# Kernel tuning notes

Hardware: AMD Instinct MI355X
Metric: run time of the kernel (lower is better)

The kernel has to match this reference:

```python
import itertools
import jax, jax.numpy as jnp
import numpy as np

ALPHA = 1e-4   # mse/conn mixing
BETA = 0.1
DMAX = 20.0
NCAP = 10.0    # costs_n_cap
PCAP = 3.0     # costs_p_cap
W3D = 64       # 3D cube window (window_3d)
W2D = 32       # 2D MALIS window (window_2d, default)


def _dilate5(mask):
    # scipy binary_dilation, default cross structuring element, 5 iterations
    m = mask.astype(bool)
    for _ in range(5):
        p = np.pad(m, 1)
        m = p[1:-1, 1:-1] | p[:-2, 1:-1] | p[2:, 1:-1] | p[1:-1, :-2] | p[1:-1, 2:]
    return m


def _label8(mask):
    # skimage.measure.label on boolean mask: 8-connectivity, background=0
    H, W = mask.shape
    lbl = np.zeros((H, W), np.int64)
    parent = {}

    def find(x):
        while parent[x] != x:
            parent[x] = parent[parent[x]]
            x = parent[x]
        return x

    nxt = 1
    for i in range(H):
        for j in range(W):
            if not mask[i, j]:
                continue
            neigh = []
            for di, dj in ((-1, -1), (-1, 0), (-1, 1), (0, -1)):
                ii, jj = i + di, j + dj
                if 0 <= ii < H and 0 <= jj < W and mask[ii, jj]:
                    neigh.append(int(lbl[ii, jj]))
            if not neigh:
                lbl[i, j] = nxt
                parent[nxt] = nxt
                nxt += 1
            else:
                m0 = min(neigh)
                lbl[i, j] = m0
                for nb in neigh:
                    ra, rb = find(m0), find(nb)
                    if ra != rb:
                        parent[max(ra, rb)] = min(ra, rb)
    out = np.zeros_like(lbl)
    remap = {}
    c = 0
    for i in range(H):
        for j in range(W):
            if lbl[i, j] > 0:
                r = find(int(lbl[i, j]))
                if r not in remap:
                    c += 1
                    remap[r] = c
                out[i, j] = remap[r]
    return out


def _malis_edge_weights(seg, n1, n2, costs, pos):
    # MALIS union-find / Kruskal maximal-spanning-tree pair counting.
    # Edges processed in descending cost order. Background (seg==0) nodes
    # are not counted. pos=1: #same-label pairs merged; pos=0: #diff-label pairs.
    n = seg.size
    parent = list(range(n))

    def find(x):
        r = x
        while parent[r] != r:
            r = parent[r]
        while parent[x] != r:
            parent[x], x = r, parent[x]
        return r

    cnt = [({int(s): 1} if s > 0 else {}) for s in seg]
    tot = [1 if s > 0 else 0 for s in seg]
    w = np.zeros(costs.shape[0], np.float32)
    for e in np.argsort(-costs, kind="stable"):
        ra, rb = find(int(n1[e])), find(int(n2[e]))
        if ra == rb:
            continue
        ca, cb = cnt[ra], cnt[rb]
        if len(ca) > len(cb):
            ra, rb, ca, cb = rb, ra, cb, ca
        same = 0
        for l, v in ca.items():
            same += v * cb.get(l, 0)
        w[e] = float(same if pos else tot[ra] * tot[rb] - same)
        for l, v in ca.items():
            cb[l] = cb.get(l, 0) + v
        tot[rb] += tot[ra]
        parent[ra] = rb
        cnt[ra] = None
    return w


def _window_weights(pred2d, tgt2d):
    # numpy MALIS node weights for a [B,1,H,W] 2D projection
    B, C, H, W = pred2d.shape
    w = W2D
    wn = np.zeros(pred2d.shape, np.float32)
    wp = np.zeros(pred2d.shape, np.float32)
    idx = np.arange(w * w).reshape(w, w)
    n1 = np.concatenate([idx[:, :-1].ravel(), idx[:-1, :].ravel()])
    n2 = np.concatenate([idx[:, 1:].ravel(), idx[1:, :].ravel()])
    nh = w * (w - 1)
    for k in range(H // w):
        for j in range(W // w):
            p = pred2d[:, :, k*w:(k+1)*w, j*w:(j+1)*w]
            t = tgt2d[:, :, k*w:(k+1)*w, j*w:(j+1)*w]
            ch = (p[:, :, :, :-1] + p[:, :, :, 1:]).reshape(B, -1)
            cv = (p[:, :, :-1, :] + p[:, :, 1:, :]).reshape(B, -1)
            costs = np.concatenate([ch, cv], 1).astype(np.float32)
            gh = (t[:, :, :, :-1] + t[:, :, :, 1:]).reshape(B, -1)
            gv = (t[:, :, :-1, :] + t[:, :, 1:, :]).reshape(B, -1)
            gt = np.concatenate([gh, gv], 1).astype(np.float32)
            costs_n = costs.copy()
            costs_p = costs.copy()
            costs_n[gt > NCAP] = NCAP
            costs_p[gt < PCAP] = 0.0
            gt = np.minimum(gt, NCAP)
            for b in range(B):
                sg = _label8(~_dilate5(t[b, 0] == 0)).ravel()
                en = _malis_edge_weights(sg, n1, n2, costs_n[b], 0)
                ep = _malis_edge_weights(sg, n1, n2, costs_p[b], 1)
                sn = en.sum()
                if sn > 0:
                    en = en / sn
                sp = ep.sum()
                if sp > 0:
                    ep = ep / sp
                en[gt[b] >= PCAP] = 0.0
                ep[gt[b] < NCAP] = 0.0
                for ew, out in ((en, wn), (ep, wp)):
                    eh = ew[:nh].reshape(w, w - 1)
                    ev = ew[nh:].reshape(w - 1, w)
                    nwt = np.zeros((w, w), np.float32)
                    nwt[:, :-1] += eh
                    nwt[:, 1:] += eh
                    nwt[:-1, :] += ev
                    nwt[1:, :] += ev
                    out[b, 0, k*w:(k+1)*w, j*w:(j+1)*w] = nwt
    return wn, wp


def _precompute(pred_np, tgt_np):
    # host-side (detached) MALIS weight maps, exactly as the torch module
    B, C, H, W, D = pred_np.shape
    items = []
    for k, j, i in itertools.product(range(H // W3D), range(W // W3D), range(D // W3D)):
        sl = (slice(None), slice(None), slice(k*W3D, (k+1)*W3D),
              slice(j*W3D, (j+1)*W3D), slice(i*W3D, (i+1)*W3D))
        pc, tc = pred_np[sl], tgt_np[sl]
        for axis in (2, 3, 4):
            wn, wp = _window_weights(pc.min(axis=axis), tc.min(axis=axis))
            items.append((k, j, i, axis, jnp.asarray(wn), jnp.asarray(wp)))
    return items


def _loss(pred, target, items):
    mse = jnp.mean((pred - target) ** 2)
    conn = jnp.float32(0.0)
    for (k, j, i, axis, wn, wp) in items:
        pc = pred[:, :, k*W3D:(k+1)*W3D, j*W3D:(j+1)*W3D, i*W3D:(i+1)*W3D]
        proj = jnp.min(pc, axis=axis)  # [B,1,64,64]
        conn = conn + jnp.sum(proj**2 * wn + BETA * (DMAX - proj)**2 * wp)
    return (mse, jnp.float32(ALPHA) * conn)


def setup_inputs() -> dict:
    # synthetic distance-transform-like volumes (zeros on 'vessel' seeds)
    rng = np.random.default_rng(0)
    B, H = 4, 128
    g = np.arange(H, dtype=np.float32)
    zz, yy, xx = np.meshgrid(g, g, g, indexing="ij")
    tgt = np.empty((B, 1, H, H, H), np.float32)
    for b in range(B):
        pts = rng.uniform(0, H, size=(24, 3)).astype(np.float32)
        d = np.full((H, H, H), np.inf, np.float32)
        for p in pts:
            d = np.minimum(d, np.sqrt((zz - p[0])**2 + (yy - p[1])**2 + (xx - p[2])**2))
        tgt[b, 0] = np.floor(np.minimum(d, DMAX))
    pred = np.clip(tgt + 0.5 * rng.standard_normal(tgt.shape).astype(np.float32), 0.0, DMAX).astype(np.float32)
    return {"pred": jnp.asarray(pred), "target": jnp.asarray(tgt)}


def reference(pred, target):
    items = _precompute(np.asarray(pred), np.asarray(target))
    return _loss(pred, target, items)
```

## Files before the change

kernel.cpp:

```cpp
#include <hip/hip_runtime.h>

#define BLOCK 256
#define NNODE 1024
#define NH    992
#define NE    1984
#define NSORT 2048
#define LMAX  12
#define CHUNK 64
#define NPASS (NE / CHUNK)

typedef unsigned long long ull;

__device__ __forceinline__ void edge_nodes(int e, int& a, int& b) {
    if (e < NH) {
        int r = e / 31;
        int c = e - r * 31;
        a = (r << 5) + c;
        b = a + 1;
    } else {
        a = e - NH;
        b = a + 32;
    }
}

__device__ __forceinline__ int find_par(unsigned short* par, int x) {
    volatile unsigned short* vp = par;
    int r = x;
    int p = vp[r];
    while (p != r) { r = p; p = vp[r]; }
    int c = x;
    while (c != r) { const int nxt = vp[c]; vp[c] = (unsigned short)r; c = nxt; }
    return r;
}

__device__ __forceinline__ int dot16x4(ull a, ull b) {
    int s  = (int)(a & 0xFFFFu)         * (int)(b & 0xFFFFu);
    s     += (int)((a >> 16) & 0xFFFFu) * (int)((b >> 16) & 0xFFFFu);
    s     += (int)((a >> 32) & 0xFFFFu) * (int)((b >> 32) & 0xFFFFu);
    s     += (int)((a >> 48) & 0xFFFFu) * (int)((b >> 48) & 0xFFFFu);
    return s;
}

__device__ __forceinline__ void cswap(unsigned int& ka, unsigned short& ia,
                                      unsigned int& kb, unsigned short& ib, bool up) {
    const bool gt = (ka > kb) || (ka == kb && ia > ib);
    if (gt == up) {
        const unsigned int  tk = ka; ka = kb; kb = tk;
        const unsigned short ti = ia; ia = ib; ib = ti;
    }
}

__global__ __launch_bounds__(BLOCK) void conn_kernel(const float* __restrict__ pred,
                                                     const float* __restrict__ tgt,
                                                     double* __restrict__ acc_ws,
                                                     int B) {
    __shared__ float          sh_p[NNODE];
    __shared__ float          sh_t[NNODE];
    __shared__ alignas(16) unsigned int   sh_key[NSORT];
    __shared__ alignas(16) unsigned short sh_idx[NSORT];
    __shared__ unsigned short sh_parent[NNODE];
    __shared__ unsigned int   sh_szto[NNODE];
    __shared__ ull            sh_cnt64[NNODE * 3];
    __shared__ unsigned char  sh_seg[NNODE];
    __shared__ int            sh_flag;
    __shared__ int            sh_L;
    __shared__ float          sh_sn;
    __shared__ double         sh_red[4];

    const int tid = threadIdx.x;
    int wg = blockIdx.x;
    const int sign = wg & 1;  wg >>= 1;
    const int b    = wg % B;  wg /= B;
    const int win  = wg & 3;  wg >>= 2;
    const int item = wg;
    const int axis_id = item % 3;
    const int cube = item / 3;
    const int ci = cube & 1;
    const int cj = (cube >> 1) & 1;
    const int ck = (cube >> 2) & 1;
    const int wk = win >> 1;
    const int wj = win & 1;

    const size_t base = (size_t)b * 2097152u;

    for (int pix = tid; pix < NNODE; pix += BLOCK) {
        const int r = pix >> 5, c = pix & 31;
        const int R = wk * 32 + r, C = wj * 32 + c;
        float pm, tm;
        if (axis_id == 2) {
            const size_t idx0 = base + (size_t)(ck * 64 + R) * 16384u + (size_t)(cj * 64 + C) * 128u + (size_t)(ci * 64);
            const float4* pp = reinterpret_cast<const float4*>(pred + idx0);
            const float4* tp = reinterpret_cast<const float4*>(tgt + idx0);
            pm = 3.4e38f; tm = 3.4e38f;
            #pragma unroll
            for (int h = 0; h < 16; ++h) {
                const float4 a = pp[h];
                const float4 t = tp[h];
                pm = fminf(pm, fminf(fminf(a.x, a.y), fminf(a.z, a.w)));
                tm = fminf(tm, fminf(fminf(t.x, t.y), fminf(t.z, t.w)));
            }
        } else {
            size_t idx0; int stride;
            if (axis_id == 0) {
                idx0 = base + (size_t)(ck * 64) * 16384u + (size_t)(cj * 64 + R) * 128u + (size_t)(ci * 64 + C);
                stride = 16384;
            } else {
                idx0 = base + (size_t)(ck * 64 + R) * 16384u + (size_t)(cj * 64) * 128u + (size_t)(ci * 64 + C);
                stride = 128;
            }
            pm = 3.4e38f; tm = 3.4e38f;
            for (int h = 0; h < 64; ++h) {
                pm = fminf(pm, pred[idx0]);
                tm = fminf(tm, tgt[idx0]);
                idx0 += (size_t)stride;
            }
        }
        sh_p[pix] = pm;
        sh_t[pix] = tm;
    }
    __syncthreads();

    unsigned char* mA = sh_seg;
    unsigned char* mB = (unsigned char*)sh_idx;
    for (int pix = tid; pix < NNODE; pix += BLOCK)
        mA[pix] = (sh_t[pix] == 0.0f) ? 1 : 0;
    __syncthreads();
    for (int it = 0; it < 5; ++it) {
        unsigned char* src = (it & 1) ? mB : mA;
        unsigned char* dst = (it & 1) ? mA : mB;
        for (int pix = tid; pix < NNODE; pix += BLOCK) {
            const int r = pix >> 5, c = pix & 31;
            unsigned char v = src[pix];
            if (r > 0)  v |= src[pix - 32];
            if (r < 31) v |= src[pix + 32];
            if (c > 0)  v |= src[pix - 1];
            if (c < 31) v |= src[pix + 1];
            dst[pix] = v;
        }
        __syncthreads();
    }
    for (int pix = tid; pix < NNODE; pix += BLOCK)
        mA[pix] = mB[pix] ^ 1;
    __syncthreads();

    for (int pix = tid; pix < NNODE; pix += BLOCK)
        sh_parent[pix] = mA[pix] ? (unsigned short)pix : (unsigned short)0xFFFF;
    __syncthreads();
    for (;;) {
        if (tid == 0) sh_flag = 0;
        __syncthreads();
        for (int pix = tid; pix < NNODE; pix += BLOCK) {
            if (!mA[pix]) continue;
            const int r = pix >> 5, c = pix & 31;
            int m = sh_parent[pix];
            #pragma unroll
            for (int d = 0; d < 8; ++d) {
                static const int dr[8] = {-1,-1,-1, 0, 0, 1, 1, 1};
                static const int dc[8] = {-1, 0, 1,-1, 1,-1, 0, 1};
                const int rr = r + dr[d], cc = c + dc[d];
                if (rr < 0 || rr > 31 || cc < 0 || cc > 31) continue;
                const int nb = (rr << 5) + cc;
                if (mA[nb]) { int v = sh_parent[nb]; if (v < m) m = v; }
            }
            while ((int)sh_parent[m] < m) m = sh_parent[m];
            if (m < (int)sh_parent[pix]) { sh_parent[pix] = (unsigned short)m; sh_flag = 1; }
        }
        __syncthreads();
        const int f = sh_flag;
        __syncthreads();
        if (f == 0) break;
    }

    if (tid == 0) sh_L = 0;
    __syncthreads();
    for (int pix = tid; pix < NNODE; pix += BLOCK) {
        if (mA[pix] && (int)sh_parent[pix] == pix) {
            const int id = atomicAdd(&sh_L, 1);
            sh_szto[pix] = (unsigned int)(id + 1);
        }
    }
    __syncthreads();
    for (int pix = tid; pix < NNODE; pix += BLOCK) {
        unsigned char s = 0;
        if (mA[pix]) {
            int lab = (int)sh_szto[sh_parent[pix]];
            if (lab > 255) lab = 255;
            s = (unsigned char)lab;
        }
        sh_seg[pix] = s;
    }
    __syncthreads();

    for (int pix = tid; pix < NNODE; pix += BLOCK) {
        sh_parent[pix] = (unsigned short)pix;
        const int s = sh_seg[pix];
        const unsigned int tot = (s > 0 && s <= LMAX) ? 1u : 0u;
        sh_szto[pix] = 1u | (tot << 16);
        ull c0 = 0, c1 = 0, c2 = 0;
        if (s >= 1 && s <= LMAX) {
            const ull bit = 1ull << (((s - 1) & 3) * 16);
            const int q = (s - 1) >> 2;
            if (q == 0) c0 = bit; else if (q == 1) c1 = bit; else c2 = bit;
        }
        sh_cnt64[pix * 3 + 0] = c0;
        sh_cnt64[pix * 3 + 1] = c1;
        sh_cnt64[pix * 3 + 2] = c2;
    }
    __syncthreads();

    unsigned int   K[8];
    unsigned short I[8];
    const int b8 = tid << 3;
    #pragma unroll
    for (int l = 0; l < 8; ++l) {
        const int e = b8 + l;
        if (e < NE) {
            int a, bb; edge_nodes(e, a, bb);
            float cost = sh_p[a] + sh_p[bb];
            const float g = sh_t[a] + sh_t[bb];
            if (sign == 0) { if (g > 10.0f) cost = 10.0f; }
            else           { if (g <  3.0f) cost = 0.0f;  }
            K[l] = ~__float_as_uint(cost);
            I[l] = (unsigned short)e;
        } else {
            K[l] = 0xFFFFFFFFu;
            I[l] = (unsigned short)0xFFFF;
        }
    }
    cswap(K[0],I[0],K[1],I[1], true );
    cswap(K[2],I[2],K[3],I[3], false);
    cswap(K[4],I[4],K[5],I[5], true );
    cswap(K[6],I[6],K[7],I[7], false);
    cswap(K[0],I[0],K[2],I[2], true );
    cswap(K[1],I[1],K[3],I[3], true );
    cswap(K[4],I[4],K[6],I[6], false);
    cswap(K[5],I[5],K[7],I[7], false);
    cswap(K[0],I[0],K[1],I[1], true );
    cswap(K[2],I[2],K[3],I[3], true );
    cswap(K[4],I[4],K[5],I[5], false);
    cswap(K[6],I[6],K[7],I[7], false);
    {
        const bool u8 = ((b8 & 8) == 0);
        cswap(K[0],I[0],K[4],I[4], u8); cswap(K[1],I[1],K[5],I[5], u8);
        cswap(K[2],I[2],K[6],I[6], u8); cswap(K[3],I[3],K[7],I[7], u8);
        cswap(K[0],I[0],K[2],I[2], u8); cswap(K[1],I[1],K[3],I[3], u8);
        cswap(K[4],I[4],K[6],I[6], u8); cswap(K[5],I[5],K[7],I[7], u8);
        cswap(K[0],I[0],K[1],I[1], u8); cswap(K[2],I[2],K[3],I[3], u8);
        cswap(K[4],I[4],K[5],I[5], u8); cswap(K[6],I[6],K[7],I[7], u8);
    }
    {
        uint4 k0, k1, iv;
        k0.x=K[0]; k0.y=K[1]; k0.z=K[2]; k0.w=K[3];
        k1.x=K[4]; k1.y=K[5]; k1.z=K[6]; k1.w=K[7];
        iv.x=(unsigned int)I[0] | ((unsigned int)I[1]<<16);
        iv.y=(unsigned int)I[2] | ((unsigned int)I[3]<<16);
        iv.z=(unsigned int)I[4] | ((unsigned int)I[5]<<16);
        iv.w=(unsigned int)I[6] | ((unsigned int)I[7]<<16);
        *reinterpret_cast<uint4*>(&sh_key[b8])     = k0;
        *reinterpret_cast<uint4*>(&sh_key[b8 + 4]) = k1;
        *reinterpret_cast<uint4*>(&sh_idx[b8])     = iv;
    }
    __syncthreads();

    for (int k = 16; k <= NSORT; k <<= 1) {
        for (int j = k >> 1; j >= 8; j >>= 1) {
            for (int i = tid; i < NSORT; i += BLOCK) {
                const int ixj = i ^ j;
                if (ixj > i) {
                    const unsigned int ka = sh_key[i], kb = sh_key[ixj];
                    const unsigned short ia = sh_idx[i], ib = sh_idx[ixj];
                    const bool gt = (ka > kb) || (ka == kb && ia > ib);
                    const bool up = ((i & k) == 0);
                    if (gt == up) {
                        sh_key[i] = kb; sh_key[ixj] = ka;
                        sh_idx[i] = ib; sh_idx[ixj] = ia;
                    }
                }
            }
            __syncthreads();
        }
        {
            const uint4 k0 = *reinterpret_cast<const uint4*>(&sh_key[b8]);
            const uint4 k1 = *reinterpret_cast<const uint4*>(&sh_key[b8 + 4]);
            const uint4 iv = *reinterpret_cast<const uint4*>(&sh_idx[b8]);
            K[0]=k0.x; K[1]=k0.y; K[2]=k0.z; K[3]=k0.w;
            K[4]=k1.x; K[5]=k1.y; K[6]=k1.z; K[7]=k1.w;
            I[0]=(unsigned short)(iv.x); I[1]=(unsigned short)(iv.x>>16);
            I[2]=(unsigned short)(iv.y); I[3]=(unsigned short)(iv.y>>16);
            I[4]=(unsigned short)(iv.z); I[5]=(unsigned short)(iv.z>>16);
            I[6]=(unsigned short)(iv.w); I[7]=(unsigned short)(iv.w>>16);
            const bool u8 = ((b8 & k) == 0);
            cswap(K[0],I[0],K[4],I[4], u8); cswap(K[1],I[1],K[5],I[5], u8);
            cswap(K[2],I[2],K[6],I[6], u8); cswap(K[3],I[3],K[7],I[7], u8);
            cswap(K[0],I[0],K[2],I[2], u8); cswap(K[1],I[1],K[3],I[3], u8);
            cswap(K[4],I[4],K[6],I[6], u8); cswap(K[5],I[5],K[7],I[7], u8);
            cswap(K[0],I[0],K[1],I[1], u8); cswap(K[2],I[2],K[3],I[3], u8);
            cswap(K[4],I[4],K[5],I[5], u8); cswap(K[6],I[6],K[7],I[7], u8);
            uint4 o0, o1, ov;
            o0.x=K[0]; o0.y=K[1]; o0.z=K[2]; o0.w=K[3];
            o1.x=K[4]; o1.y=K[5]; o1.z=K[6]; o1.w=K[7];
            ov.x=(unsigned int)I[0] | ((unsigned int)I[1]<<16);
            ov.y=(unsigned int)I[2] | ((unsigned int)I[3]<<16);
            ov.z=(unsigned int)I[4] | ((unsigned int)I[5]<<16);
            ov.w=(unsigned int)I[6] | ((unsigned int)I[7]<<16);
            *reinterpret_cast<uint4*>(&sh_key[b8])     = o0;
            *reinterpret_cast<uint4*>(&sh_key[b8 + 4]) = o1;
            *reinterpret_cast<uint4*>(&sh_idx[b8])     = ov;
        }
        __syncthreads();
    }

    for (int e = tid; e < NE; e += BLOCK) sh_key[e] = 0u;
    __syncthreads();

    if (tid < 64) {
        const int lane = tid;
        for (int pass = 0; pass < NPASS; ++pass) {
            const int e = sh_idx[pass * CHUNK + lane];
            int a, bb; edge_nodes(e, a, bb);
            int ra = find_par(sh_parent, a);
            int rb = find_par(sh_parent, bb);
            ull m = __ballot(ra != rb);
            while (m) {
                const int i = (int)__builtin_ctzll(m);
                m &= m - 1;
                const unsigned int pack = (unsigned int)ra | ((unsigned int)rb << 10) | ((unsigned int)e << 20);
                const unsigned int pk = (unsigned int)__shfl((int)pack, i);
                const int ra_i = (int)(pk & 1023u);
                const int rb_i = (int)((pk >> 10) & 1023u);
                if (ra_i == rb_i) continue;
                const int se = (int)(pk >> 20);
                const unsigned int xa = sh_szto[ra_i], xb = sh_szto[rb_i];
                const ull a0 = sh_cnt64[ra_i * 3 + 0];
                const ull a1 = sh_cnt64[ra_i * 3 + 1];
                const ull a2 = sh_cnt64[ra_i * 3 + 2];
                const ull b0 = sh_cnt64[rb_i * 3 + 0];
                const ull b1 = sh_cnt64[rb_i * 3 + 1];
                const ull b2 = sh_cnt64[rb_i * 3 + 2];
                const int ta = (int)(xa >> 16), tb = (int)(xb >> 16);
                const int same = dot16x4(a0, b0) + dot16x4(a1, b1) + dot16x4(a2, b2);
                const int wv = sign ? same : (ta * tb - same);
                const int big = ((xa & 0xFFFFu) > (xb & 0xFFFFu));
                const int rs = big ? ra_i : rb_i;
                const int rl = big ? rb_i : ra_i;
                if (lane == 0) {
                    sh_key[se] = __float_as_uint((float)wv);
                    sh_cnt64[rs * 3 + 0] = a0 + b0;
                    sh_cnt64[rs * 3 + 1] = a1 + b1;
                    sh_cnt64[rs * 3 + 2] = a2 + b2;
                    sh_szto[rs] = xa + xb;
                    sh_parent[rl] = (unsigned short)rs;
                }
                if (ra == rl) ra = rs;
                if (rb == rl) rb = rs;
            }
        }
    }
    __syncthreads();

    {
        float part = 0.0f;
        for (int e = tid; e < NE; e += BLOCK) part += __uint_as_float(sh_key[e]);
        for (int off = 32; off > 0; off >>= 1) part += __shfl_down(part, off, 64);
        if ((tid & 63) == 0) sh_red[tid >> 6] = (double)part;
        __syncthreads();
        if (tid == 0) sh_sn = (float)(sh_red[0] + sh_red[1] + sh_red[2] + sh_red[3]);
        __syncthreads();
    }
    const float sn = sh_sn;

    double acc = 0.0;
    for (int pix = tid; pix < NNODE; pix += BLOCK) {
        const int r = pix >> 5, c = pix & 31;
        float nw = 0.0f;
        if (c < 31) { const int e = r * 31 + c;
            float v = __uint_as_float(sh_key[e]); if (sn > 0.0f) v = v / sn;
            const float g = sh_t[pix] + sh_t[pix + 1];
            if (sign == 0) { if (g >= 3.0f) v = 0.0f; } else { if (g < 10.0f) v = 0.0f; }
            nw += v; }
        if (c > 0)  { const int e = r * 31 + c - 1;
            float v = __uint_as_float(sh_key[e]); if (sn > 0.0f) v = v / sn;
            const float g = sh_t[pix - 1] + sh_t[pix];
            if (sign == 0) { if (g >= 3.0f) v = 0.0f; } else { if (g < 10.0f) v = 0.0f; }
            nw += v; }
        if (r < 31) { const int e = NH + pix;
            float v = __uint_as_float(sh_key[e]); if (sn > 0.0f) v = v / sn;
            const float g = sh_t[pix] + sh_t[pix + 32];
            if (sign == 0) { if (g >= 3.0f) v = 0.0f; } else { if (g < 10.0f) v = 0.0f; }
            nw += v; }
        if (r > 0)  { const int e = NH + pix - 32;
            float v = __uint_as_float(sh_key[e]); if (sn > 0.0f) v = v / sn;
            const float g = sh_t[pix - 32] + sh_t[pix];
            if (sign == 0) { if (g >= 3.0f) v = 0.0f; } else { if (g < 10.0f) v = 0.0f; }
            nw += v; }
        const float p = sh_p[pix];
        float term;
        if (sign == 0) {
            term = (p * p) * nw;
        } else {
            const float d = 20.0f - p;
            term = (0.1f * (d * d)) * nw;
        }
        acc += (double)term;
    }
    for (int off = 32; off > 0; off >>= 1) acc += __shfl_down(acc, off, 64);
    if ((tid & 63) == 0) sh_red[tid >> 6] = acc;
    __syncthreads();
    if (tid == 0)
        atomicAdd(&acc_ws[1], sh_red[0] + sh_red[1] + sh_red[2] + sh_red[3]);
}

__global__ __launch_bounds__(BLOCK) void mse_kernel(const float* __restrict__ pred,
                                                    const float* __restrict__ tgt,
                                                    double* __restrict__ acc_ws,
                                                    long n) {
    double acc = 0.0;
    for (long i = (long)blockIdx.x * BLOCK + threadIdx.x; i < n; i += (long)gridDim.x * BLOCK) {
        const float d = pred[i] - tgt[i];
        acc += (double)(d * d);
    }
    for (int off = 32; off > 0; off >>= 1) acc += __shfl_down(acc, off, 64);
    __shared__ double red[4];
    if ((threadIdx.x & 63) == 0) red[threadIdx.x >> 6] = acc;
    __syncthreads();
    if (threadIdx.x == 0)
        atomicAdd(&acc_ws[0], red[0] + red[1] + red[2] + red[3]);
}

__global__ void fin_kernel(const double* __restrict__ acc_ws, float* __restrict__ out, long n) {
    if (threadIdx.x == 0 && blockIdx.x == 0) {
        out[0] = (float)(acc_ws[0] / (double)n);
        out[1] = (float)(acc_ws[1] * (double)1e-4f);
    }
}

extern "C" void kernel_launch(void* const* d_in, const int* in_sizes, int n_in,
                              void* d_out, int out_size, void* d_ws, size_t ws_size,
                              hipStream_t stream) {
    const float* pred = (const float*)d_in[0];
    const float* tgt  = (const float*)d_in[1];
    float* out = (float*)d_out;
    double* acc = (double*)d_ws;

    const long n = (long)in_sizes[0];
    const int  B = (int)(n / 2097152);

    hipMemsetAsync(d_ws, 0, 2 * sizeof(double), stream);
    mse_kernel<<<1024, BLOCK, 0, stream>>>(pred, tgt, acc, n);
    conn_kernel<<<192 * B, BLOCK, 0, stream>>>(pred, tgt, acc, B);
    fin_kernel<<<1, 64, 0, stream>>>(acc, out, n);
}
```

Measured before the change: 568.8 us.

## Vectorize strided projection loads, remap block order, compact bitonic pairs, pipeline merge loop

```diff
diff --git a/kernel.cpp b/kernel.cpp
--- a/kernel.cpp
+++ b/kernel.cpp
@@ -54,8 +54,8 @@
                                                      const float* __restrict__ tgt,
                                                      double* __restrict__ acc_ws,
                                                      int B) {
-    __shared__ float          sh_p[NNODE];
-    __shared__ float          sh_t[NNODE];
+    __shared__ alignas(16) float          sh_p[NNODE];
+    __shared__ alignas(16) float          sh_t[NNODE];
     __shared__ alignas(16) unsigned int   sh_key[NSORT];
     __shared__ alignas(16) unsigned short sh_idx[NSORT];
     __shared__ unsigned short sh_parent[NNODE];
@@ -69,7 +69,8 @@
 
     const int tid = threadIdx.x;
     int wg = blockIdx.x;
-    const int sign = wg & 1;  wg >>= 1;
+    const int sign = (wg >> 3) & 1;
+    wg = (wg & 7) | ((wg >> 4) << 3);
     const int b    = wg % B;  wg /= B;
     const int win  = wg & 3;  wg >>= 2;
     const int item = wg;
@@ -83,15 +84,14 @@
 
     const size_t base = (size_t)b * 2097152u;
 
-    for (int pix = tid; pix < NNODE; pix += BLOCK) {
-        const int r = pix >> 5, c = pix & 31;
-        const int R = wk * 32 + r, C = wj * 32 + c;
-        float pm, tm;
-        if (axis_id == 2) {
+    if (axis_id == 2) {
+        for (int pix = tid; pix < NNODE; pix += BLOCK) {
+            const int r = pix >> 5, c = pix & 31;
+            const int R = wk * 32 + r, C = wj * 32 + c;
             const size_t idx0 = base + (size_t)(ck * 64 + R) * 16384u + (size_t)(cj * 64 + C) * 128u + (size_t)(ci * 64);
             const float4* pp = reinterpret_cast<const float4*>(pred + idx0);
             const float4* tp = reinterpret_cast<const float4*>(tgt + idx0);
-            pm = 3.4e38f; tm = 3.4e38f;
+            float pm = 3.4e38f, tm = 3.4e38f;
             #pragma unroll
             for (int h = 0; h < 16; ++h) {
                 const float4 a = pp[h];
@@ -99,24 +99,35 @@
                 pm = fminf(pm, fminf(fminf(a.x, a.y), fminf(a.z, a.w)));
                 tm = fminf(tm, fminf(fminf(t.x, t.y), fminf(t.z, t.w)));
             }
+            sh_p[pix] = pm;
+            sh_t[pix] = tm;
+        }
+    } else {
+        const int r  = tid >> 3;
+        const int c0 = (tid & 7) << 2;
+        const int R = wk * 32 + r, C = wj * 32 + c0;
+        size_t idx0; int hstride;
+        if (axis_id == 0) {
+            idx0 = base + (size_t)(ck * 64) * 16384u + (size_t)(cj * 64 + R) * 128u + (size_t)(ci * 64 + C);
+            hstride = 16384;
         } else {
-            size_t idx0; int stride;
-            if (axis_id == 0) {
-                idx0 = base + (size_t)(ck * 64) * 16384u + (size_t)(cj * 64 + R) * 128u + (size_t)(ci * 64 + C);
-                stride = 16384;
-            } else {
-                idx0 = base + (size_t)(ck * 64 + R) * 16384u + (size_t)(cj * 64) * 128u + (size_t)(ci * 64 + C);
-                stride = 128;
-            }
-            pm = 3.4e38f; tm = 3.4e38f;
-            for (int h = 0; h < 64; ++h) {
-                pm = fminf(pm, pred[idx0]);
-                tm = fminf(tm, tgt[idx0]);
-                idx0 += (size_t)stride;
-            }
-        }
-        sh_p[pix] = pm;
-        sh_t[pix] = tm;
+            idx0 = base + (size_t)(ck * 64 + R) * 16384u + (size_t)(cj * 64) * 128u + (size_t)(ci * 64 + C);
+            hstride = 128;
+        }
+        float4 pm = make_float4(3.4e38f, 3.4e38f, 3.4e38f, 3.4e38f);
+        float4 tm = pm;
+        #pragma unroll 8
+        for (int h = 0; h < 64; ++h) {
+            const float4 a  = *reinterpret_cast<const float4*>(pred + idx0);
+            const float4 t4 = *reinterpret_cast<const float4*>(tgt + idx0);
+            pm.x = fminf(pm.x, a.x);  pm.y = fminf(pm.y, a.y);
+            pm.z = fminf(pm.z, a.z);  pm.w = fminf(pm.w, a.w);
+            tm.x = fminf(tm.x, t4.x); tm.y = fminf(tm.y, t4.y);
+            tm.z = fminf(tm.z, t4.z); tm.w = fminf(tm.w, t4.w);
+            idx0 += (size_t)hstride;
+        }
+        *reinterpret_cast<float4*>(&sh_p[(r << 5) + c0]) = pm;
+        *reinterpret_cast<float4*>(&sh_t[(r << 5) + c0]) = tm;
     }
     __syncthreads();
 
@@ -264,17 +275,16 @@
 
     for (int k = 16; k <= NSORT; k <<= 1) {
         for (int j = k >> 1; j >= 8; j >>= 1) {
-            for (int i = tid; i < NSORT; i += BLOCK) {
-                const int ixj = i ^ j;
-                if (ixj > i) {
-                    const unsigned int ka = sh_key[i], kb = sh_key[ixj];
-                    const unsigned short ia = sh_idx[i], ib = sh_idx[ixj];
-                    const bool gt = (ka > kb) || (ka == kb && ia > ib);
-                    const bool up = ((i & k) == 0);
-                    if (gt == up) {
-                        sh_key[i] = kb; sh_key[ixj] = ka;
-                        sh_idx[i] = ib; sh_idx[ixj] = ia;
-                    }
+            for (int p = tid; p < (NSORT >> 1); p += BLOCK) {
+                const int i   = ((p & ~(j - 1)) << 1) | (p & (j - 1));
+                const int ixj = i | j;
+                const unsigned int ka = sh_key[i], kb = sh_key[ixj];
+                const unsigned short ia = sh_idx[i], ib = sh_idx[ixj];
+                const bool gt = (ka > kb) || (ka == kb && ia > ib);
+                const bool up = ((i & k) == 0);
+                if (gt == up) {
+                    sh_key[i] = kb; sh_key[ixj] = ka;
+                    sh_idx[i] = ib; sh_idx[ixj] = ia;
                 }
             }
             __syncthreads();
@@ -321,38 +331,60 @@
             int ra = find_par(sh_parent, a);
             int rb = find_par(sh_parent, bb);
             ull m = __ballot(ra != rb);
-            while (m) {
-                const int i = (int)__builtin_ctzll(m);
-                m &= m - 1;
-                const unsigned int pack = (unsigned int)ra | ((unsigned int)rb << 10) | ((unsigned int)e << 20);
-                const unsigned int pk = (unsigned int)__shfl((int)pack, i);
+            if (m == 0) continue;
+            int i0 = (int)__builtin_ctzll(m); m &= m - 1;
+            unsigned int pk = (unsigned int)__shfl(
+                (int)((unsigned int)ra | ((unsigned int)rb << 10) | ((unsigned int)e << 20)), i0);
+            for (;;) {
                 const int ra_i = (int)(pk & 1023u);
                 const int rb_i = (int)((pk >> 10) & 1023u);
-                if (ra_i == rb_i) continue;
-                const int se = (int)(pk >> 20);
-                const unsigned int xa = sh_szto[ra_i], xb = sh_szto[rb_i];
-                const ull a0 = sh_cnt64[ra_i * 3 + 0];
-                const ull a1 = sh_cnt64[ra_i * 3 + 1];
-                const ull a2 = sh_cnt64[ra_i * 3 + 2];
-                const ull b0 = sh_cnt64[rb_i * 3 + 0];
-                const ull b1 = sh_cnt64[rb_i * 3 + 1];
-                const ull b2 = sh_cnt64[rb_i * 3 + 2];
-                const int ta = (int)(xa >> 16), tb = (int)(xb >> 16);
-                const int same = dot16x4(a0, b0) + dot16x4(a1, b1) + dot16x4(a2, b2);
-                const int wv = sign ? same : (ta * tb - same);
-                const int big = ((xa & 0xFFFFu) > (xb & 0xFFFFu));
-                const int rs = big ? ra_i : rb_i;
-                const int rl = big ? rb_i : ra_i;
-                if (lane == 0) {
-                    sh_key[se] = __float_as_uint((float)wv);
-                    sh_cnt64[rs * 3 + 0] = a0 + b0;
-                    sh_cnt64[rs * 3 + 1] = a1 + b1;
-                    sh_cnt64[rs * 3 + 2] = a2 + b2;
-                    sh_szto[rs] = xa + xb;
-                    sh_parent[rl] = (unsigned short)rs;
+                const bool live = (ra_i != rb_i);
+                unsigned int xa = 0, xb = 0;
+                ull a0 = 0, a1 = 0, a2 = 0, b0 = 0, b1 = 0, b2 = 0;
+                if (live) {
+                    xa = sh_szto[ra_i]; xb = sh_szto[rb_i];
+                    a0 = sh_cnt64[ra_i * 3 + 0];
+                    a1 = sh_cnt64[ra_i * 3 + 1];
+                    a2 = sh_cnt64[ra_i * 3 + 2];
+                    b0 = sh_cnt64[rb_i * 3 + 0];
+                    b1 = sh_cnt64[rb_i * 3 + 1];
+                    b2 = sh_cnt64[rb_i * 3 + 2];
                 }
-                if (ra == rl) ra = rs;
-                if (rb == rl) rb = rs;
+                const bool have_next = (m != 0);
+                unsigned int pk_next = 0;
+                if (have_next) {
+                    const int ni = (int)__builtin_ctzll(m); m &= m - 1;
+                    pk_next = (unsigned int)__shfl(
+                        (int)((unsigned int)ra | ((unsigned int)rb << 10) | ((unsigned int)e << 20)), ni);
+                }
+                if (live) {
+                    const int ta = (int)(xa >> 16), tb = (int)(xb >> 16);
+                    const int same = dot16x4(a0, b0) + dot16x4(a1, b1) + dot16x4(a2, b2);
+                    const int wv = sign ? same : (ta * tb - same);
+                    const int big = ((xa & 0xFFFFu) > (xb & 0xFFFFu));
+                    const int rs = big ? ra_i : rb_i;
+                    const int rl = big ? rb_i : ra_i;
+                    const int se = (int)(pk >> 20);
+                    if (lane == 0) {
+                        sh_key[se] = __float_as_uint((float)wv);
+                        sh_cnt64[rs * 3 + 0] = a0 + b0;
+                        sh_cnt64[rs * 3 + 1] = a1 + b1;
+                        sh_cnt64[rs * 3 + 2] = a2 + b2;
+                        sh_szto[rs] = xa + xb;
+                        sh_parent[rl] = (unsigned short)rs;
+                    }
+                    if (ra == rl) ra = rs;
+                    if (rb == rl) rb = rs;
+                    if (have_next) {
+                        unsigned int r1 = pk_next & 1023u;
+                        unsigned int r2 = (pk_next >> 10) & 1023u;
+                        if (r1 == (unsigned int)rl) r1 = (unsigned int)rs;
+                        if (r2 == (unsigned int)rl) r2 = (unsigned int)rs;
+                        pk_next = r1 | (r2 << 10) | (pk_next & 0xFFF00000u);
+                    }
+                }
+                if (!have_next) break;
+                pk = pk_next;
             }
         }
     }
```

Result: no change. 562.6 us (-1.1%).
